# Kernel tuning notes

Hardware: AMD Instinct MI355X
Metric: run time of the kernel (lower is better)

The kernel has to match this reference:

```python
import jax, jax.numpy as jnp
import numpy as np

N_HEADS = 16


def setup_inputs() -> dict:
    key = jax.random.key(0)
    bs, width, length = 2, 3072, 2048  # width = 3 * n_heads * ch, ch = 64
    qkv = jax.random.normal(key, (bs, width, length), dtype=jnp.float32)
    return {"qkv": qkv}


def reference(qkv):
    bs, width, length = qkv.shape
    ch = width // (3 * N_HEADS)
    # per-head layout within width is [q(ch), k(ch), v(ch)]
    qkv_h = qkv.reshape(bs * N_HEADS, 3 * ch, length)
    q, k, v = jnp.split(qkv_h, 3, axis=1)  # each [bs*H, ch, L]
    scale = 1.0 / jnp.sqrt(jnp.sqrt(jnp.asarray(ch, dtype=qkv.dtype)))
    # scores: [bs*H, L_q, L_k]
    weight = jnp.einsum('bct,bcs->bts', q * scale, k * scale)
    weight = jax.nn.softmax(weight.astype(jnp.float32), axis=-1).astype(qkv.dtype)
    a = jnp.einsum('bts,bcs->bct', weight, v)  # [bs*H, ch, L]
    return a.reshape(bs, -1, length)
```

## Files before the change

### kernel.cpp

```cpp
#include <hip/hip_runtime.h>
#include <hip/hip_bf16.h>
#include <stdint.h>

typedef float f32x4 __attribute__((ext_vector_type(4)));
typedef float f32x16 __attribute__((ext_vector_type(16)));
typedef __bf16 bf16x8 __attribute__((ext_vector_type(8)));
typedef uint32_t u32;
typedef u32 u32x4 __attribute__((ext_vector_type(4)));

#define SCALE 0.35355339059327378f
#define SCALE2 0.42466090014400953f
#define LOG2E 1.4426950408889634f

#if __has_builtin(__builtin_amdgcn_exp2f)
__device__ __forceinline__ float exp2fast(float x) { return __builtin_amdgcn_exp2f(x); }
#else
__device__ __forceinline__ float exp2fast(float x) { return exp2f(x); }
#endif

__device__ __forceinline__ u32 packbf2(float a, float b) {
  u32 ua = __builtin_bit_cast(u32, a);
  u32 ub = __builtin_bit_cast(u32, b);
  ua = (ua + 0x7fffu + ((ua >> 16) & 1u)) >> 16;
  ub = (ub + 0x7fffu + ((ub >> 16) & 1u)) >> 16;
  return ua | (ub << 16);
}
__device__ __forceinline__ unsigned short tobf(float a) {
  u32 ua = __builtin_bit_cast(u32, a);
  return (unsigned short)((ua + 0x7fffu + ((ua >> 16) & 1u)) >> 16);
}
__device__ __forceinline__ u32 pk2(float a, float b) {
  unsigned short lo = __builtin_bit_cast(unsigned short, (__bf16)a);
  unsigned short hi = __builtin_bit_cast(unsigned short, (__bf16)b);
  return (u32)lo | ((u32)hi << 16);
}
__device__ __forceinline__ int swz(int row, int col) {
  return row * 64 + (col ^ ((row & 7) << 3));
}
__device__ __forceinline__ void gload16(const void* g, void* l) {
  __builtin_amdgcn_global_load_lds((const __attribute__((address_space(1))) void*)g,
                                   (__attribute__((address_space(3))) void*)l, 16, 0, 0);
}
__device__ __forceinline__ f32x16 zero16() {
  f32x16 z;
#pragma unroll
  for (int i = 0; i < 16; ++i) z[i] = 0.f;
  return z;
}

__global__ __launch_bounds__(256) void prep_kernel(const float* __restrict__ qkv,
                                                   unsigned short* __restrict__ ws) {
  __shared__ unsigned short tq[64 * 64];
  __shared__ unsigned short tk[64 * 64];
  const int tid = threadIdx.x;
  const int bid = blockIdx.x;
  const int bh = bid >> 5;
  const int tile = bid & 31;
  const int b = bh >> 4, h = bh & 15;
  const float* hq = qkv + ((size_t)b * 3072 + (size_t)h * 192) * 2048;
  const int s0 = tile * 64;

  {
    const int c = tid >> 2;
    const int jj = (tid & 3) * 16;
    const float* qp = hq + (size_t)c * 2048 + s0 + jj;
    const float* kp = qp + 64 * 2048;
    const float* vp = qp + 128 * 2048;
    unsigned short* vout = ws + (size_t)64 * 131072 + (size_t)bh * 131072 +
                           (size_t)c * 2048 + s0 + jj;
    u32 vbuf[8];
#pragma unroll
    for (int u = 0; u < 4; ++u) {
      f32x4 fq = *(const f32x4*)(qp + u * 4);
      f32x4 fk = *(const f32x4*)(kp + u * 4);
      f32x4 fv = *(const f32x4*)(vp + u * 4);
#pragma unroll
      for (int e = 0; e < 4; ++e) {
        int s = jj + u * 4 + e;
        int sw = swz(s, c);
        tq[sw] = tobf(fq[e] * SCALE2);
        tk[sw] = tobf(fk[e] * SCALE2);
      }
      vbuf[2 * u]     = packbf2(fv[0], fv[1]);
      vbuf[2 * u + 1] = packbf2(fv[2], fv[3]);
    }
    *(u32x4*)(vout)     = *(u32x4*)&vbuf[0];
    *(u32x4*)(vout + 8) = *(u32x4*)&vbuf[4];
  }
  __syncthreads();
  {
    const int s = tid >> 2;
    const int c0 = (tid & 3) * 16;
    const int ch0 = (((c0 >> 3) ^ (s & 7)) << 3);
    const int ch1 = ((((c0 >> 3) + 1) ^ (s & 7)) << 3);
    size_t ob = (size_t)bh * 131072 + (size_t)(s0 + s) * 64 + c0;
    unsigned short* qout = ws + ob;
    unsigned short* kout = ws + (size_t)32 * 131072 + ob;
    *(u32x4*)qout       = *(u32x4*)&tq[s * 64 + ch0];
    *(u32x4*)(qout + 8) = *(u32x4*)&tq[s * 64 + ch1];
    *(u32x4*)kout       = *(u32x4*)&tk[s * 64 + ch0];
    *(u32x4*)(kout + 8) = *(u32x4*)&tk[s * 64 + ch1];
  }
}

__global__ __launch_bounds__(512, 4) void attn10_kernel(const unsigned short* __restrict__ ws,
                                                        float* __restrict__ out) {
  __shared__ __align__(16) char smem[66560];

  const int tid  = threadIdx.x;
  const int lane = tid & 63;
  const int wv   = tid >> 6;
  const int w4   = wv & 3;
  const int grp  = wv >> 2;
  const int l31  = lane & 31;
  const int hi   = lane >> 5;

  const int bid = blockIdx.x;
  const int bh  = (bid & 7) * 4 + ((bid >> 3) >> 4);
  const int qb  = (bid >> 3) & 15;
  const int b = bh >> 4, h = bh & 15;

  const unsigned short* Qs = ws + (size_t)bh * 131072;
  const unsigned short* Ks = ws + (size_t)32 * 131072 + (size_t)bh * 131072;
  const unsigned short* Vs = ws + (size_t)64 * 131072 + (size_t)bh * 131072;

  bf16x8 qB[4];
#pragma unroll
  for (int kc = 0; kc < 4; ++kc)
    qB[kc] = *(const bf16x8*)(Qs + (size_t)(qb * 128 + w4 * 32 + l31) * 64 + kc * 16 + hi * 8);

  const int srow = lane >> 3;
  const int sch  = (lane & 7) ^ srow;
  const char* kg = (const char*)Ks + (size_t)(w4 * 16 + srow) * 128  + sch * 16;
  const char* vg = (const char*)Vs + (size_t)(w4 * 16 + srow) * 4096 + sch * 16;
  char* kbase = smem + grp * 16384;
  char* vbase = smem + 32768 + grp * 16384;
  char* kd = kbase + w4 * 2048;
  char* vd = vbase + w4 * 2048;

  f32x16 oacc0 = zero16(), oacc1 = zero16();
  float lrun = 0.f;

  {
    const char* kgn = kg + (size_t)grp * 8192;
    const char* vgn = vg + (size_t)grp * 128;
    gload16(kgn,         kd);
    gload16(kgn + 1024,  kd + 1024);
    gload16(vgn,         vd);
    gload16(vgn + 32768, vd + 1024);
  }

  for (int it = 0; it < 16; ++it) {
    const int cur = it & 1;
    __syncthreads();
    if (it < 15) {
      const int stn = 2 * (it + 1) + grp;
      const char* kgn = kg + (size_t)stn * 8192;
      const char* vgn = vg + (size_t)stn * 128;
      char* kdn = kd + (cur ^ 1) * 8192;
      char* vdn = vd + (cur ^ 1) * 8192;
      gload16(kgn,         kdn);
      gload16(kgn + 1024,  kdn + 1024);
      gload16(vgn,         vdn);
      gload16(vgn + 32768, vdn + 1024);
    }

    const unsigned short* kt = (const unsigned short*)(kbase + cur * 8192);
    f32x16 a0 = zero16(), a1 = zero16();
    const int xr = (l31 & 7);
    __builtin_amdgcn_s_setprio(1);
#pragma unroll
    for (int kc = 0; kc < 4; ++kc) {
      int chs = ((kc * 2 + hi) ^ xr) << 3;
      bf16x8 kA0 = *(const bf16x8*)(kt + l31 * 64 + chs);
      bf16x8 kA1 = *(const bf16x8*)(kt + (32 + l31) * 64 + chs);
      a0 = __builtin_amdgcn_mfma_f32_32x32x16_bf16(kA0, qB[kc], a0, 0, 0, 0);
      a1 = __builtin_amdgcn_mfma_f32_32x32x16_bf16(kA1, qB[kc], a1, 0, 0, 0);
    }
    __builtin_amdgcn_s_setprio(0);

#pragma unroll
    for (int i = 0; i < 16; ++i) a0[i] = exp2fast(a0[i]);
#pragma unroll
    for (int i = 0; i < 16; ++i) a1[i] = exp2fast(a1[i]);
    {
      f32x16 s01 = a0 + a1;
      f32x4 s4;
#pragma unroll
      for (int i = 0; i < 4; ++i)
        s4[i] = (s01[i] + s01[i + 4]) + (s01[i + 8] + s01[i + 12]);
      lrun += (s4[0] + s4[1]) + (s4[2] + s4[3]);
    }

    bf16x8 pB[4];
#pragma unroll
    for (int sc = 0; sc < 4; ++sc) {
      const f32x16& src = (sc < 2) ? a0 : a1;
      const int rb = (sc & 1) * 8;
      u32 c01 = pk2(src[rb + 0], src[rb + 1]);
      u32 c23 = pk2(src[rb + 2], src[rb + 3]);
      u32 c45 = pk2(src[rb + 4], src[rb + 5]);
      u32 c67 = pk2(src[rb + 6], src[rb + 7]);
      asm volatile("v_permlane32_swap_b32 %0, %1" : "+v"(c01), "+v"(c45));
      asm volatile("v_permlane32_swap_b32 %0, %1" : "+v"(c23), "+v"(c67));
      u32x4 w = {c01, c23, c45, c67};
      pB[sc] = __builtin_bit_cast(bf16x8, w);
    }

    const unsigned short* vt = (const unsigned short*)(vbase + cur * 8192);
    __builtin_amdgcn_s_setprio(1);
#pragma unroll
    for (int sc = 0; sc < 4; ++sc) {
      int chs = ((sc * 2 + hi) ^ xr) << 3;
      bf16x8 vA0 = *(const bf16x8*)(vt + l31 * 64 + chs);
      bf16x8 vA1 = *(const bf16x8*)(vt + (32 + l31) * 64 + chs);
      oacc0 = __builtin_amdgcn_mfma_f32_32x32x16_bf16(vA0, pB[sc], oacc0, 0, 0, 0);
      oacc1 = __builtin_amdgcn_mfma_f32_32x32x16_bf16(vA1, pB[sc], oacc1, 0, 0, 0);
    }
    __builtin_amdgcn_s_setprio(0);
  }

  float lfull = lrun + __shfl_xor(lrun, 32);
  __syncthreads();
  float* s_O = (float*)smem;
  float* s_l = (float*)(smem + 65536);
  if (grp == 1) {
    float* O1 = s_O + w4 * 2048;
#pragma unroll
    for (int r = 0; r < 16; ++r) {
      int c = (r & 3) + 8 * (r >> 2) + 4 * hi;
      O1[c * 32 + l31]        = oacc0[r];
      O1[(c + 32) * 32 + l31] = oacc1[r];
    }
    if (hi == 0) s_l[w4 * 32 + l31] = lfull;
  }
  __syncthreads();
  if (grp == 0) {
    float inv = 1.0f / (lfull + s_l[w4 * 32 + l31]);
    const float* O1 = s_O + w4 * 2048;
    float* outp = out + ((size_t)b * 1024 + (size_t)h * 64) * 2048;
    const int t = qb * 128 + w4 * 32 + l31;
#pragma unroll
    for (int r = 0; r < 16; ++r) {
      int c = (r & 3) + 8 * (r >> 2) + 4 * hi;
      outp[(size_t)c * 2048 + t]        = (oacc0[r] + O1[c * 32 + l31]) * inv;
      outp[(size_t)(c + 32) * 2048 + t] = (oacc1[r] + O1[(c + 32) * 32 + l31]) * inv;
    }
  }
}

__global__ __launch_bounds__(256) void qkv_attn_kernel(const float* __restrict__ qkv,
                                                       float* __restrict__ out) {
  __shared__ __align__(16) unsigned short s_kt[64 * 64];
  __shared__ __align__(16) unsigned short s_v [64 * 64];
  __shared__ __align__(16) unsigned short s_qp[128 * 64];

  const int tid  = threadIdx.x;
  const int lane = tid & 63;
  const int wv   = tid >> 6;
  const int l15  = lane & 15;
  const int lg   = lane >> 4;

  int bid = blockIdx.x;
  int bh  = (bid & 7) * 4 + ((bid >> 3) >> 4);
  int qb  = (bid >> 3) & 15;
  int b = bh >> 4, h = bh & 15;
  const float* __restrict__ hq = qkv + ((size_t)b * 3072 + (size_t)h * 192) * 2048;
  const int q0 = qb * 128;

  {
    int c  = (tid & 31) * 2;
    int tq = tid >> 5;
    const float* r0 = hq + (size_t)c * 2048 + q0;
    const float* r1 = r0 + 2048;
#pragma unroll
    for (int j = 0; j < 4; ++j) {
      int t4 = tq * 16 + j * 4;
      f32x4 f0 = *(const f32x4*)(r0 + t4);
      f32x4 f1 = *(const f32x4*)(r1 + t4);
#pragma unroll
      for (int e = 0; e < 4; ++e) {
        int t = t4 + e;
        ((u32*)s_qp)[swz(t, c) >> 1] = packbf2(f0[e] * SCALE, f1[e] * SCALE);
      }
    }
  }
  __syncthreads();

  bf16x8 qA[2][2];
#pragma unroll
  for (int tf = 0; tf < 2; ++tf)
#pragma unroll
    for (int kc = 0; kc < 2; ++kc) {
      int t  = wv * 32 + tf * 16 + l15;
      int c0 = kc * 32 + lg * 8;
      qA[tf][kc] = *(const bf16x8*)&s_qp[swz(t, c0)];
    }

  const f32x4 zf = {0.f, 0.f, 0.f, 0.f};
  f32x4 oacc[2][4];
#pragma unroll
  for (int tf = 0; tf < 2; ++tf)
#pragma unroll
    for (int cs = 0; cs < 4; ++cs) oacc[tf][cs] = zf;
  float mrun[2][4], lrun[2][4];
#pragma unroll
  for (int tf = 0; tf < 2; ++tf)
#pragma unroll
    for (int r = 0; r < 4; ++r) { mrun[tf][r] = -1e30f; lrun[tf][r] = 0.f; }

  const int pw = wv * 2048;

  for (int st = 0; st < 32; ++st) {
    const int s0g = st * 64;
    __syncthreads();
    {
      int c  = (tid & 31) * 2;
      int tq = tid >> 5;
      const float* r0 = hq + (size_t)(64 + c) * 2048 + s0g;
      const float* r1 = r0 + 2048;
#pragma unroll
      for (int j = 0; j < 2; ++j) {
        int s4 = tq * 8 + j * 4;
        f32x4 f0 = *(const f32x4*)(r0 + s4);
        f32x4 f1 = *(const f32x4*)(r1 + s4);
#pragma unroll
        for (int e = 0; e < 4; ++e)
          ((u32*)s_kt)[swz(s4 + e, c) >> 1] = packbf2(f0[e] * SCALE, f1[e] * SCALE);
      }
    }
    {
      int c  = tid >> 2;
      int sq = tid & 3;
      const float* rv = hq + (size_t)(128 + c) * 2048 + s0g;
#pragma unroll
      for (int j = 0; j < 4; ++j) {
        int s4 = sq * 16 + j * 4;
        f32x4 f = *(const f32x4*)(rv + s4);
        int si = swz(c, s4) >> 1;
        ((u32*)s_v)[si]     = packbf2(f[0], f[1]);
        ((u32*)s_v)[si + 1] = packbf2(f[2], f[3]);
      }
    }
    __syncthreads();

    f32x4 acc[2][4];
#pragma unroll
    for (int tf = 0; tf < 2; ++tf)
#pragma unroll
      for (int ss = 0; ss < 4; ++ss) acc[tf][ss] = zf;
#pragma unroll
    for (int kc = 0; kc < 2; ++kc) {
#pragma unroll
      for (int ss = 0; ss < 4; ++ss) {
        int srow = ss * 16 + l15;
        int c0   = kc * 32 + lg * 8;
        bf16x8 kB = *(const bf16x8*)&s_kt[swz(srow, c0)];
#pragma unroll
        for (int tf = 0; tf < 2; ++tf)
          acc[tf][ss] = __builtin_amdgcn_mfma_f32_16x16x32_bf16(qA[tf][kc], kB, acc[tf][ss], 0, 0, 0);
      }
    }

#pragma unroll
    for (int tf = 0; tf < 2; ++tf) {
#pragma unroll
      for (int r = 0; r < 4; ++r) {
        float tm = fmaxf(fmaxf(acc[tf][0][r], acc[tf][1][r]),
                         fmaxf(acc[tf][2][r], acc[tf][3][r]));
#pragma unroll
        for (int off = 1; off < 16; off <<= 1) tm = fmaxf(tm, __shfl_xor(tm, off));
        float mold = mrun[tf][r];
        float mnew = fmaxf(mold, tm);
        float rs   = exp2f((mold - mnew) * LOG2E);
        mrun[tf][r] = mnew;
        int t = tf * 16 + lg * 4 + r;
        float psum = 0.f;
#pragma unroll
        for (int ss = 0; ss < 4; ++ss) {
          float p = exp2f((acc[tf][ss][r] - mnew) * LOG2E);
          psum += p;
          s_qp[pw + swz(t, ss * 16 + l15)] = tobf(p);
        }
        lrun[tf][r] = lrun[tf][r] * rs + psum;
#pragma unroll
        for (int cs = 0; cs < 4; ++cs) oacc[tf][cs][r] *= rs;
      }
    }

    bf16x8 pA[2][2];
#pragma unroll
    for (int tf = 0; tf < 2; ++tf)
#pragma unroll
      for (int kc = 0; kc < 2; ++kc) {
        int t  = tf * 16 + l15;
        int s0 = kc * 32 + lg * 8;
        pA[tf][kc] = *(const bf16x8*)&s_qp[pw + swz(t, s0)];
      }
#pragma unroll
    for (int cs = 0; cs < 4; ++cs) {
#pragma unroll
      for (int kc = 0; kc < 2; ++kc) {
        int crow = cs * 16 + l15;
        int s0   = kc * 32 + lg * 8;
        bf16x8 vB = *(const bf16x8*)&s_v[swz(crow, s0)];
#pragma unroll
        for (int tf = 0; tf < 2; ++tf)
          oacc[tf][cs] = __builtin_amdgcn_mfma_f32_16x16x32_bf16(pA[tf][kc], vB, oacc[tf][cs], 0, 0, 0);
      }
    }
  }

  float* outp = out + ((size_t)b * 1024 + (size_t)h * 64) * 2048;
#pragma unroll
  for (int tf = 0; tf < 2; ++tf) {
    f32x4 invv;
#pragma unroll
    for (int r = 0; r < 4; ++r) {
      float ls = lrun[tf][r];
#pragma unroll
      for (int off = 1; off < 16; off <<= 1) ls += __shfl_xor(ls, off);
      invv[r] = 1.0f / ls;
    }
#pragma unroll
    for (int cs = 0; cs < 4; ++cs) {
      int c = cs * 16 + l15;
      float* po = outp + (size_t)c * 2048 + q0 + wv * 32 + tf * 16 + lg * 4;
      f32x4 o = oacc[tf][cs] * invv;
      *(f32x4*)po = o;
    }
  }
}

extern "C" void kernel_launch(void* const* d_in, const int* in_sizes, int n_in,
                              void* d_out, int out_size, void* d_ws, size_t ws_size,
                              hipStream_t stream) {
  (void)in_sizes; (void)n_in; (void)out_size;
  const float* qkv = (const float*)d_in[0];
  float* outp = (float*)d_out;
  const size_t need = (size_t)96 * 131072 * 2;
  if (ws_size >= need && d_ws != nullptr) {
    unsigned short* ws = (unsigned short*)d_ws;
    prep_kernel<<<dim3(1024), dim3(256), 0, stream>>>(qkv, ws);
    attn10_kernel<<<dim3(512), dim3(512), 0, stream>>>(ws, outp);
  } else {
    qkv_attn_kernel<<<dim3(512), dim3(256), 0, stream>>>(qkv, outp);
  }
}
```

Before: 63.22 us.

## Halve attention block to 4 waves, each computing two 32-query tiles

```diff
diff --git a/kernel.cpp b/kernel.cpp
--- a/kernel.cpp
+++ b/kernel.cpp
@@ -103,17 +103,18 @@
   }
 }
 
-__global__ __launch_bounds__(512, 4) void attn10_kernel(const unsigned short* __restrict__ ws,
-                                                        float* __restrict__ out) {
+__global__ __launch_bounds__(256, 2) void attn6_kernel(const unsigned short* __restrict__ ws,
+                                                       float* __restrict__ out) {
   __shared__ __align__(16) char smem[66560];
 
   const int tid  = threadIdx.x;
   const int lane = tid & 63;
   const int wv   = tid >> 6;
-  const int w4   = wv & 3;
-  const int grp  = wv >> 2;
+  const int slot = wv & 1;
+  const int grp  = wv >> 1;
   const int l31  = lane & 31;
   const int hi   = lane >> 5;
+  const int xr   = l31 & 7;
 
   const int bid = blockIdx.x;
   const int bh  = (bid & 7) * 4 + ((bid >> 3) >> 4);
@@ -124,127 +125,158 @@
   const unsigned short* Ks = ws + (size_t)32 * 131072 + (size_t)bh * 131072;
   const unsigned short* Vs = ws + (size_t)64 * 131072 + (size_t)bh * 131072;
 
-  bf16x8 qB[4];
-#pragma unroll
-  for (int kc = 0; kc < 4; ++kc)
-    qB[kc] = *(const bf16x8*)(Qs + (size_t)(qb * 128 + w4 * 32 + l31) * 64 + kc * 16 + hi * 8);
+  bf16x8 qBA[4], qBB[4];
+#pragma unroll
+  for (int kc = 0; kc < 4; ++kc) {
+    const unsigned short* qp = Qs + (size_t)(qb * 128 + slot * 64 + l31) * 64 + kc * 16 + hi * 8;
+    qBA[kc] = *(const bf16x8*)qp;
+    qBB[kc] = *(const bf16x8*)(qp + 32 * 64);
+  }
 
   const int srow = lane >> 3;
   const int sch  = (lane & 7) ^ srow;
-  const char* kg = (const char*)Ks + (size_t)(w4 * 16 + srow) * 128  + sch * 16;
-  const char* vg = (const char*)Vs + (size_t)(w4 * 16 + srow) * 4096 + sch * 16;
-  char* kbase = smem + grp * 16384;
-  char* vbase = smem + 32768 + grp * 16384;
-  char* kd = kbase + w4 * 2048;
-  char* vd = vbase + w4 * 2048;
-
-  f32x16 oacc0 = zero16(), oacc1 = zero16();
-  float lrun = 0.f;
-
-  {
-    const char* kgn = kg + (size_t)grp * 8192;
-    const char* vgn = vg + (size_t)grp * 128;
-    gload16(kgn,         kd);
-    gload16(kgn + 1024,  kd + 1024);
-    gload16(vgn,         vd);
-    gload16(vgn + 32768, vd + 1024);
-  }
-
+  const char* kg = (const char*)Ks + (size_t)slot * 4096 + (size_t)srow * 128 + sch * 16 + (size_t)grp * 8192;
+  const char* vg = (const char*)Vs + (size_t)slot * 131072 + (size_t)srow * 4096 + sch * 16 + (size_t)grp * 128;
+  char* kd = smem + grp * 16384 + slot * 4096;
+  char* vd = smem + 32768 + grp * 16384 + slot * 4096;
+
+  auto STAGE = [&](int it, int buf) {
+    const char* kgn = kg + (size_t)it * 16384;
+    const char* vgn = vg + (size_t)it * 256;
+    char* kdn = kd + buf * 8192;
+    char* vdn = vd + buf * 8192;
+#pragma unroll
+    for (int j = 0; j < 4; ++j) {
+      gload16(kgn + j * 1024,           kdn + j * 1024);
+      gload16(vgn + (size_t)j * 32768,  vdn + j * 1024);
+    }
+  };
+
+  f32x16 oA0 = zero16(), oA1 = zero16(), oB0 = zero16(), oB1 = zero16();
+  float lrunA = 0.f, lrunB = 0.f;
+
+  STAGE(0, 0);
+
+#pragma unroll 1
   for (int it = 0; it < 16; ++it) {
     const int cur = it & 1;
     __syncthreads();
-    if (it < 15) {
-      const int stn = 2 * (it + 1) + grp;
-      const char* kgn = kg + (size_t)stn * 8192;
-      const char* vgn = vg + (size_t)stn * 128;
-      char* kdn = kd + (cur ^ 1) * 8192;
-      char* vdn = vd + (cur ^ 1) * 8192;
-      gload16(kgn,         kdn);
-      gload16(kgn + 1024,  kdn + 1024);
-      gload16(vgn,         vdn);
-      gload16(vgn + 32768, vdn + 1024);
-    }
-
-    const unsigned short* kt = (const unsigned short*)(kbase + cur * 8192);
-    f32x16 a0 = zero16(), a1 = zero16();
-    const int xr = (l31 & 7);
+    if (it < 15) STAGE(it + 1, cur ^ 1);
+
+    const unsigned short* kt = (const unsigned short*)(smem + grp * 16384 + cur * 8192);
+    f32x16 aA0 = zero16(), aA1 = zero16(), aB0 = zero16(), aB1 = zero16();
     __builtin_amdgcn_s_setprio(1);
 #pragma unroll
     for (int kc = 0; kc < 4; ++kc) {
       int chs = ((kc * 2 + hi) ^ xr) << 3;
       bf16x8 kA0 = *(const bf16x8*)(kt + l31 * 64 + chs);
       bf16x8 kA1 = *(const bf16x8*)(kt + (32 + l31) * 64 + chs);
-      a0 = __builtin_amdgcn_mfma_f32_32x32x16_bf16(kA0, qB[kc], a0, 0, 0, 0);
-      a1 = __builtin_amdgcn_mfma_f32_32x32x16_bf16(kA1, qB[kc], a1, 0, 0, 0);
+      aA0 = __builtin_amdgcn_mfma_f32_32x32x16_bf16(kA0, qBA[kc], aA0, 0, 0, 0);
+      aA1 = __builtin_amdgcn_mfma_f32_32x32x16_bf16(kA1, qBA[kc], aA1, 0, 0, 0);
+      aB0 = __builtin_amdgcn_mfma_f32_32x32x16_bf16(kA0, qBB[kc], aB0, 0, 0, 0);
+      aB1 = __builtin_amdgcn_mfma_f32_32x32x16_bf16(kA1, qBB[kc], aB1, 0, 0, 0);
     }
     __builtin_amdgcn_s_setprio(0);
 
 #pragma unroll
-    for (int i = 0; i < 16; ++i) a0[i] = exp2fast(a0[i]);
-#pragma unroll
-    for (int i = 0; i < 16; ++i) a1[i] = exp2fast(a1[i]);
+    for (int i = 0; i < 16; ++i) aA0[i] = exp2fast(aA0[i]);
+#pragma unroll
+    for (int i = 0; i < 16; ++i) aA1[i] = exp2fast(aA1[i]);
+#pragma unroll
+    for (int i = 0; i < 16; ++i) aB0[i] = exp2fast(aB0[i]);
+#pragma unroll
+    for (int i = 0; i < 16; ++i) aB1[i] = exp2fast(aB1[i]);
     {
-      f32x16 s01 = a0 + a1;
-      f32x4 s4;
-#pragma unroll
-      for (int i = 0; i < 4; ++i)
-        s4[i] = (s01[i] + s01[i + 4]) + (s01[i + 8] + s01[i + 12]);
-      lrun += (s4[0] + s4[1]) + (s4[2] + s4[3]);
-    }
-
-    bf16x8 pB[4];
+      f32x16 sA = aA0 + aA1, sB = aB0 + aB1;
+      f32x4 s4A, s4B;
+#pragma unroll
+      for (int i = 0; i < 4; ++i) {
+        s4A[i] = (sA[i] + sA[i + 4]) + (sA[i + 8] + sA[i + 12]);
+        s4B[i] = (sB[i] + sB[i + 4]) + (sB[i + 8] + sB[i + 12]);
+      }
+      lrunA += (s4A[0] + s4A[1]) + (s4A[2] + s4A[3]);
+      lrunB += (s4B[0] + s4B[1]) + (s4B[2] + s4B[3]);
+    }
+
+    bf16x8 pBA[4], pBB[4];
 #pragma unroll
     for (int sc = 0; sc < 4; ++sc) {
-      const f32x16& src = (sc < 2) ? a0 : a1;
+      const f32x16& sa = (sc < 2) ? aA0 : aA1;
+      const f32x16& sb = (sc < 2) ? aB0 : aB1;
       const int rb = (sc & 1) * 8;
-      u32 c01 = pk2(src[rb + 0], src[rb + 1]);
-      u32 c23 = pk2(src[rb + 2], src[rb + 3]);
-      u32 c45 = pk2(src[rb + 4], src[rb + 5]);
-      u32 c67 = pk2(src[rb + 6], src[rb + 7]);
-      asm volatile("v_permlane32_swap_b32 %0, %1" : "+v"(c01), "+v"(c45));
-      asm volatile("v_permlane32_swap_b32 %0, %1" : "+v"(c23), "+v"(c67));
-      u32x4 w = {c01, c23, c45, c67};
-      pB[sc] = __builtin_bit_cast(bf16x8, w);
-    }
-
-    const unsigned short* vt = (const unsigned short*)(vbase + cur * 8192);
+      {
+        u32 c01 = pk2(sa[rb + 0], sa[rb + 1]);
+        u32 c23 = pk2(sa[rb + 2], sa[rb + 3]);
+        u32 c45 = pk2(sa[rb + 4], sa[rb + 5]);
+        u32 c67 = pk2(sa[rb + 6], sa[rb + 7]);
+        asm volatile("v_permlane32_swap_b32 %0, %1" : "+v"(c01), "+v"(c45));
+        asm volatile("v_permlane32_swap_b32 %0, %1" : "+v"(c23), "+v"(c67));
+        u32x4 w = {c01, c23, c45, c67};
+        pBA[sc] = __builtin_bit_cast(bf16x8, w);
+      }
+      {
+        u32 c01 = pk2(sb[rb + 0], sb[rb + 1]);
+        u32 c23 = pk2(sb[rb + 2], sb[rb + 3]);
+        u32 c45 = pk2(sb[rb + 4], sb[rb + 5]);
+        u32 c67 = pk2(sb[rb + 6], sb[rb + 7]);
+        asm volatile("v_permlane32_swap_b32 %0, %1" : "+v"(c01), "+v"(c45));
+        asm volatile("v_permlane32_swap_b32 %0, %1" : "+v"(c23), "+v"(c67));
+        u32x4 w = {c01, c23, c45, c67};
+        pBB[sc] = __builtin_bit_cast(bf16x8, w);
+      }
+    }
+
+    const unsigned short* vt = (const unsigned short*)(smem + 32768 + grp * 16384 + cur * 8192);
     __builtin_amdgcn_s_setprio(1);
 #pragma unroll
     for (int sc = 0; sc < 4; ++sc) {
       int chs = ((sc * 2 + hi) ^ xr) << 3;
       bf16x8 vA0 = *(const bf16x8*)(vt + l31 * 64 + chs);
       bf16x8 vA1 = *(const bf16x8*)(vt + (32 + l31) * 64 + chs);
-      oacc0 = __builtin_amdgcn_mfma_f32_32x32x16_bf16(vA0, pB[sc], oacc0, 0, 0, 0);
-      oacc1 = __builtin_amdgcn_mfma_f32_32x32x16_bf16(vA1, pB[sc], oacc1, 0, 0, 0);
+      oA0 = __builtin_amdgcn_mfma_f32_32x32x16_bf16(vA0, pBA[sc], oA0, 0, 0, 0);
+      oA1 = __builtin_amdgcn_mfma_f32_32x32x16_bf16(vA1, pBA[sc], oA1, 0, 0, 0);
+      oB0 = __builtin_amdgcn_mfma_f32_32x32x16_bf16(vA0, pBB[sc], oB0, 0, 0, 0);
+      oB1 = __builtin_amdgcn_mfma_f32_32x32x16_bf16(vA1, pBB[sc], oB1, 0, 0, 0);
     }
     __builtin_amdgcn_s_setprio(0);
   }
 
-  float lfull = lrun + __shfl_xor(lrun, 32);
+  float lfA = lrunA + __shfl_xor(lrunA, 32);
+  float lfB = lrunB + __shfl_xor(lrunB, 32);
   __syncthreads();
   float* s_O = (float*)smem;
   float* s_l = (float*)(smem + 65536);
   if (grp == 1) {
-    float* O1 = s_O + w4 * 2048;
+    float* OA = s_O + (slot * 2 + 0) * 2048;
+    float* OB = s_O + (slot * 2 + 1) * 2048;
 #pragma unroll
     for (int r = 0; r < 16; ++r) {
       int c = (r & 3) + 8 * (r >> 2) + 4 * hi;
-      O1[c * 32 + l31]        = oacc0[r];
-      O1[(c + 32) * 32 + l31] = oacc1[r];
-    }
-    if (hi == 0) s_l[w4 * 32 + l31] = lfull;
+      OA[c * 32 + l31]        = oA0[r];
+      OA[(c + 32) * 32 + l31] = oA1[r];
+      OB[c * 32 + l31]        = oB0[r];
+      OB[(c + 32) * 32 + l31] = oB1[r];
+    }
+    if (hi == 0) {
+      s_l[(slot * 2 + 0) * 32 + l31] = lfA;
+      s_l[(slot * 2 + 1) * 32 + l31] = lfB;
+    }
   }
   __syncthreads();
   if (grp == 0) {
-    float inv = 1.0f / (lfull + s_l[w4 * 32 + l31]);
-    const float* O1 = s_O + w4 * 2048;
+    float invA = 1.0f / (lfA + s_l[(slot * 2 + 0) * 32 + l31]);
+    float invB = 1.0f / (lfB + s_l[(slot * 2 + 1) * 32 + l31]);
+    const float* OA = s_O + (slot * 2 + 0) * 2048;
+    const float* OB = s_O + (slot * 2 + 1) * 2048;
     float* outp = out + ((size_t)b * 1024 + (size_t)h * 64) * 2048;
-    const int t = qb * 128 + w4 * 32 + l31;
+    const int tA = qb * 128 + slot * 64 + l31;
 #pragma unroll
     for (int r = 0; r < 16; ++r) {
       int c = (r & 3) + 8 * (r >> 2) + 4 * hi;
-      outp[(size_t)c * 2048 + t]        = (oacc0[r] + O1[c * 32 + l31]) * inv;
-      outp[(size_t)(c + 32) * 2048 + t] = (oacc1[r] + O1[(c + 32) * 32 + l31]) * inv;
+      outp[(size_t)c * 2048 + tA]             = (oA0[r] + OA[c * 32 + l31]) * invA;
+      outp[(size_t)(c + 32) * 2048 + tA]      = (oA1[r] + OA[(c + 32) * 32 + l31]) * invA;
+      outp[(size_t)c * 2048 + tA + 32]        = (oB0[r] + OB[c * 32 + l31]) * invB;
+      outp[(size_t)(c + 32) * 2048 + tA + 32] = (oB1[r] + OB[(c + 32) * 32 + l31]) * invB;
     }
   }
 }
@@ -442,7 +474,7 @@
   if (ws_size >= need && d_ws != nullptr) {
     unsigned short* ws = (unsigned short*)d_ws;
     prep_kernel<<<dim3(1024), dim3(256), 0, stream>>>(qkv, ws);
-    attn10_kernel<<<dim3(512), dim3(512), 0, stream>>>(ws, outp);
+    attn6_kernel<<<dim3(512), dim3(256), 0, stream>>>(ws, outp);
   } else {
     qkv_attn_kernel<<<dim3(512), dim3(256), 0, stream>>>(qkv, outp);
   }
```

New measurement: 65.59 us. 3.8% more time.
